# Kernel optimization log

Hardware: AMD Instinct MI355X
Metric: run time of the kernel (lower is better)

The kernel has to match this reference:

```python
import jax, jax.numpy as jnp
import numpy as np

TOP_K = 4  # top_k_neighbors from __init__


def setup_inputs() -> dict:
    key = jax.random.key(0)
    k1, k2, k3, k4 = jax.random.split(key, 4)
    R, B, D, N = 256, 64, 512, 16
    h = jax.random.normal(k1, (R, B, D), dtype=jnp.float32)
    nbrs = jax.random.randint(k2, (R, N), 0, R, dtype=jnp.int32)
    W_msg = jax.random.normal(k3, (D, D), dtype=jnp.float32) * 0.02
    b_msg = jnp.zeros((D,), dtype=jnp.float32)
    W_merge = jax.random.normal(k4, (D, 2 * D), dtype=jnp.float32) * 0.02
    b_merge = jnp.zeros((D,), dtype=jnp.float32)
    return {
        "h_by_region": h,
        "neighbor_indices": nbrs,
        "W_msg": W_msg,
        "b_msg": b_msg,
        "W_merge": W_merge,
        "b_merge": b_merge,
    }


def reference(h_by_region, neighbor_indices, W_msg, b_msg, W_merge, b_merge):
    # h_by_region: [R, B, D]; neighbor_indices: [R, N] int32
    R, B, D = h_by_region.shape
    h = h_by_region
    # sim(r, j) = mean over (B, D) of h[r] * h[j]. Compute the full Gram once
    # ([R, R], tiny) instead of materializing [R, N, B, D] just for sims.
    G = jnp.einsum('rbd,sbd->rs', h, h) / (B * D)
    sims = jnp.take_along_axis(G, neighbor_indices, axis=1)           # [R, N]
    _, top = jax.lax.top_k(sims, TOP_K)                               # [R, K]
    sel = jnp.take_along_axis(neighbor_indices, top, axis=1)          # [R, K]
    # Gather selected neighbor states, project to messages, average over K.
    h_sel = h[sel]                                                    # [R, K, B, D]
    msgs = jnp.einsum('rkbd,ed->rkbe', h_sel, W_msg) + b_msg          # [R, K, B, D]
    m = msgs.mean(axis=1)                                             # [R, B, D]
    cat = jnp.concatenate([h, m], axis=-1)                            # [R, B, 2D]
    out = jnp.einsum('rbf,ef->rbe', cat, W_merge) + b_merge           # [R, B, D]
    avg_fanin = jnp.float32(TOP_K)  # every region keeps exactly top_k neighbors
    return out, avg_fanin
```

## Files before the change

### kernel.cpp

```cpp
#include <hip/hip_runtime.h>
#include <hip/hip_bf16.h>

#define R_ 256
#define B_ 64
#define D_ 512
#define N_ 16
#define K_ 4
#define RBD (B_ * D_)
#define OUT_ELEMS (R_ * B_ * D_)
#define M_TOT (R_ * B_)
#define GSLICES 64
#define GPAIRS 10
#define GBLK (GSLICES * GPAIRS)

typedef __attribute__((address_space(1))) unsigned int g_u32;
typedef __attribute__((address_space(3))) unsigned int l_u32;
using f32x4 = __attribute__((ext_vector_type(4))) float;
using f16x8 = __attribute__((ext_vector_type(8))) _Float16;
using f16x4 = __attribute__((ext_vector_type(4))) _Float16;

__constant__ int kBx[GPAIRS] = {0, 0, 0, 0, 1, 1, 1, 2, 2, 3};
__constant__ int kBy[GPAIRS] = {0, 1, 2, 3, 1, 2, 3, 2, 3, 3};

__global__ __launch_bounds__(256, 4) void gramx_kernel(
    const float* __restrict__ h, const float* __restrict__ Wm,
    const float* __restrict__ Wmsg, _Float16* __restrict__ A16,
    float* __restrict__ Cp, float* __restrict__ W2p) {
  __shared__ char smem[32768];
  const int t = threadIdx.x;
  const int bid = blockIdx.x;

  if (bid >= GBLK) {
    const int gid = bid - GBLK;
    const int db = (gid & 15) * 32;
    const int eb = ((gid >> 4) & 15) * 32;
    const int kc = gid >> 8;
    float(*As)[33] = (float(*)[33])smem;
    float(*Bs)[33] = (float(*)[33])(smem + 32 * 33 * 4);
    const int tx = t % 16, ty = t / 16;
    const int lr = t / 8;
    const int lc = (t % 8) * 4;
    float a00 = 0.f, a01 = 0.f, a10 = 0.f, a11 = 0.f;
    for (int c0 = kc * 128; c0 < kc * 128 + 128; c0 += 32) {
      float4 av = *(const float4*)&Wm[(size_t)(eb + lr) * 1024 + 512 + c0 + lc];
      float4 bv = *(const float4*)&Wmsg[(size_t)(c0 + lr) * 512 + db + lc];
      As[lr][lc + 0] = av.x; As[lr][lc + 1] = av.y;
      As[lr][lc + 2] = av.z; As[lr][lc + 3] = av.w;
      Bs[lr][lc + 0] = bv.x; Bs[lr][lc + 1] = bv.y;
      Bs[lr][lc + 2] = bv.z; Bs[lr][lc + 3] = bv.w;
      __syncthreads();
#pragma unroll
      for (int kk = 0; kk < 32; kk++) {
        float x0 = As[2 * ty + 0][kk], x1 = As[2 * ty + 1][kk];
        float y0 = Bs[kk][2 * tx + 0], y1 = Bs[kk][2 * tx + 1];
        a00 += x0 * y0; a01 += x0 * y1;
        a10 += x1 * y0; a11 += x1 * y1;
      }
      __syncthreads();
    }
    float* base = W2p + (size_t)kc * 512 * 512;
    base[(size_t)(eb + 2 * ty + 0) * 512 + db + 2 * tx + 0] = a00;
    base[(size_t)(eb + 2 * ty + 0) * 512 + db + 2 * tx + 1] = a01;
    base[(size_t)(eb + 2 * ty + 1) * 512 + db + 2 * tx + 0] = a10;
    base[(size_t)(eb + 2 * ty + 1) * 512 + db + 2 * tx + 1] = a11;
    return;
  }

  const int work = (bid & 7) * (GBLK / 8) + (bid >> 3);
  const int s = work / GPAIRS;
  const int pr = work % GPAIRS;
  const int bx = kBx[pr];
  const int by = kBy[pr];
  const int I = bx * 64;
  const int J = by * 64;
  const bool duty = (bx == by);
  const int lane = t & 63;
  const int w = t >> 6;
  char* sHiI = smem;
  char* sHiJ = smem + 8192;
  char* sLoJ = smem + 16384;
  char* sLoI = smem + 24576;
  const int wm = w >> 1, wn = w & 1;
  const int rlane = lane & 15;
  const int kq = lane >> 4;

  f32x4 c1[2][2] = {};
  f32x4 c2[2][2] = {};
  f32x4 c3[2][2] = {};

  const float* hI = h + (size_t)I * RBD + (size_t)s * 512;
  const float* hJ = h + (size_t)J * RBD + (size_t)s * 512;
  const int frow = t >> 4;
  const int fc4 = t & 15;

  float4 rI[4], rJ[4];
#pragma unroll
  for (int u = 0; u < 4; ++u) {
    const int row = u * 16 + frow;
    rI[u] = *(const float4*)&hI[(size_t)row * RBD + fc4 * 4];
    rJ[u] = *(const float4*)&hJ[(size_t)row * RBD + fc4 * 4];
  }

  for (int kt = 0; kt < 8; ++kt) {
    if (kt) __syncthreads();
#pragma unroll
    for (int u = 0; u < 4; ++u) {
      const int row = u * 16 + frow;
      const int boff =
          row * 128 + (((fc4 >> 1) ^ (row & 7)) << 4) + (fc4 & 1) * 8;
      float4 vI = rI[u];
      f16x4 hiI = {(_Float16)vI.x, (_Float16)vI.y, (_Float16)vI.z,
                   (_Float16)vI.w};
      f16x4 loI = {(_Float16)(vI.x - (float)hiI[0]),
                   (_Float16)(vI.y - (float)hiI[1]),
                   (_Float16)(vI.z - (float)hiI[2]),
                   (_Float16)(vI.w - (float)hiI[3])};
      *(f16x4*)(sHiI + boff) = hiI;
      *(f16x4*)(sLoI + boff) = loI;
      float4 vJ = rJ[u];
      f16x4 hiJ = {(_Float16)vJ.x, (_Float16)vJ.y, (_Float16)vJ.z,
                   (_Float16)vJ.w};
      f16x4 loJ = {(_Float16)(vJ.x - (float)hiJ[0]),
                   (_Float16)(vJ.y - (float)hiJ[1]),
                   (_Float16)(vJ.z - (float)hiJ[2]),
                   (_Float16)(vJ.w - (float)hiJ[3])};
      *(f16x4*)(sHiJ + boff) = hiJ;
      *(f16x4*)(sLoJ + boff) = loJ;
      if (duty)
        *(f16x4*)&A16[(size_t)(J + row) * RBD + (size_t)s * 512 + kt * 64 +
                      fc4 * 4] = hiJ;
    }
    __syncthreads();
    if (kt < 7) {
#pragma unroll
      for (int u = 0; u < 4; ++u) {
        const int row = u * 16 + frow;
        rI[u] =
            *(const float4*)&hI[(size_t)row * RBD + (kt + 1) * 64 + fc4 * 4];
        rJ[u] =
            *(const float4*)&hJ[(size_t)row * RBD + (kt + 1) * 64 + fc4 * 4];
      }
    }
#pragma unroll
    for (int ks = 0; ks < 2; ++ks) {
      f16x8 ai[2], li[2], bj[2], lj[2];
#pragma unroll
      for (int i = 0; i < 2; ++i) {
        const int row = wm * 32 + i * 16 + rlane;
        const int slot = (ks * 4 + kq) ^ (row & 7);
        ai[i] = *(const f16x8*)(sHiI + row * 128 + slot * 16);
        li[i] = *(const f16x8*)(sLoI + row * 128 + slot * 16);
      }
#pragma unroll
      for (int j = 0; j < 2; ++j) {
        const int row = wn * 32 + j * 16 + rlane;
        const int slot = (ks * 4 + kq) ^ (row & 7);
        bj[j] = *(const f16x8*)(sHiJ + row * 128 + slot * 16);
        lj[j] = *(const f16x8*)(sLoJ + row * 128 + slot * 16);
      }
#pragma unroll
      for (int i = 0; i < 2; ++i)
#pragma unroll
        for (int j = 0; j < 2; ++j) {
          c1[i][j] = __builtin_amdgcn_mfma_f32_16x16x32_f16(ai[i], bj[j],
                                                            c1[i][j], 0, 0, 0);
          c2[i][j] = __builtin_amdgcn_mfma_f32_16x16x32_f16(ai[i], lj[j],
                                                            c2[i][j], 0, 0, 0);
          c3[i][j] = __builtin_amdgcn_mfma_f32_16x16x32_f16(li[i], bj[j],
                                                            c3[i][j], 0, 0, 0);
        }
    }
  }

  f32x4 cs[2][2];
#pragma unroll
  for (int i = 0; i < 2; ++i)
#pragma unroll
    for (int j = 0; j < 2; ++j)
      cs[i][j] = c1[i][j] + c2[i][j] + c3[i][j];

#pragma unroll
  for (int i = 0; i < 2; ++i) {
#pragma unroll
    for (int reg = 0; reg < 4; ++reg) {
      const int gr = I + wm * 32 + i * 16 + kq * 4 + reg;
      const size_t base = ((size_t)s * 256 + gr) * 256 + J + wn * 32 + rlane;
#pragma unroll
      for (int j = 0; j < 2; ++j) Cp[base + j * 16] = cs[i][j][reg];
    }
  }
  if (!duty) {
#pragma unroll
    for (int i = 0; i < 2; ++i)
#pragma unroll
      for (int j = 0; j < 2; ++j) {
        const int gc = J + wn * 32 + j * 16 + rlane;
        const int gr0 = I + wm * 32 + i * 16 + kq * 4;
        *(f32x4*)&Cp[((size_t)s * 256 + gc) * 256 + gr0] = cs[i][j];
      }
  }
}

__global__ __launch_bounds__(256) void fin_kernel(
    const float* __restrict__ Cp, const int* __restrict__ nbrs,
    const float* __restrict__ W2p, const float* __restrict__ Wm,
    const float* __restrict__ b_msg, const float* __restrict__ b_merge,
    int* __restrict__ sel, float* __restrict__ fanin,
    _Float16* __restrict__ W16, float* __restrict__ bias_eff) {
  const int bx = blockIdx.x;
  const int t = threadIdx.x;
  if (bx < 256) {
    const int r = bx;
    __shared__ float sims_all[256];
    __shared__ int nb_s[N_];
    const float* base = Cp + (size_t)r * 256 + t;
    float acc = 0.f;
#pragma unroll 8
    for (int s = 0; s < GSLICES; ++s) acc += base[(size_t)s * 65536];
    sims_all[t] = acc;
    if (t < N_) nb_s[t] = nbrs[r * N_ + t];
    __syncthreads();
    if (t == 0) {
      float sims_s[N_];
#pragma unroll
      for (int n = 0; n < N_; ++n) sims_s[n] = sims_all[nb_s[n]];
      unsigned used = 0;
#pragma unroll
      for (int k = 0; k < K_; k++) {
        float best = -3.0e38f;
        int bi = 0;
        for (int nn = 0; nn < N_; nn++) {
          if (used & (1u << nn)) continue;
          float vv = sims_s[nn];
          if (vv > best) { best = vv; bi = nn; }
        }
        used |= 1u << bi;
        sel[r * K_ + k] = nb_s[bi];
      }
      if (r == 0) *fanin = 4.0f;
    }
  } else if (bx < 1280) {
    const int i = (bx - 256) * 256 + t;
    const int e = i >> 9;
    const int d = i & 511;
    float acc = 0.f;
#pragma unroll
    for (int kc = 0; kc < 4; ++kc)
      acc += W2p[(size_t)kc * 512 * 512 + (size_t)e * 512 + d];
    W16[(size_t)e * 1024 + 512 + d] = (_Float16)acc;
  } else if (bx < 1536) {
    const int i = (bx - 1280) * 256 + t;
    const int e = i >> 7;
    const int c4 = (i & 127) * 4;
    float4 v = *(const float4*)&Wm[(size_t)e * 1024 + c4];
    f16x4 o = {(_Float16)v.x, (_Float16)v.y, (_Float16)v.z, (_Float16)v.w};
    *(f16x4*)&W16[(size_t)e * 1024 + c4] = o;
  } else {
    const int e = (bx - 1536) * 256 + t;
    const float4* bp = (const float4*)b_msg;
    const float4* wp = (const float4*)&Wm[(size_t)e * 1024 + 512];
    float acc = 0.f;
    for (int c = 0; c < 128; c++) {
      float4 b4 = bp[c], w4 = wp[c];
      acc += b4.x * w4.x + b4.y * w4.y + b4.z * w4.z + b4.w * w4.w;
    }
    bias_eff[e] = acc + b_merge[e];
  }
}

__global__ __launch_bounds__(256, 4) void mfma_gemm_kernel(
    const _Float16* __restrict__ A16, const int* __restrict__ sel,
    const _Float16* __restrict__ W16, const float* __restrict__ bias,
    float* __restrict__ out) {
  const int t = threadIdx.x;
  const int lane = t & 63;
  const int w = t >> 6;
  const int bid = blockIdx.x;
  const int work = (bid & 7) * 128 + (bid >> 3);
  const int eb = (work & 3) * 128;
  const int my = work >> 2;
  const int m0 = my * 64;
  __shared__ char smemA[64 * 128];
  __shared__ char smemW[128 * 128];
  __shared__ int sel_s[4];
  const int wm = w >> 1, wn = w & 1;
  const int rlane = lane & 15;
  const int kq = lane >> 4;

  if (t < 4) sel_s[t] = sel[my * 4 + t];
  __syncthreads();

  f32x4 acc[2][4] = {};

  const char* Ab = (const char*)A16;
  const char* Wb = (const char*)W16;
  const _Float16* g0 = A16 + (size_t)sel_s[0] * RBD;
  const _Float16* g1 = A16 + (size_t)sel_s[1] * RBD;
  const _Float16* g2 = A16 + (size_t)sel_s[2] * RBD;
  const _Float16* g3 = A16 + (size_t)sel_s[3] * RBD;

  for (int kt = 0; kt < 16; ++kt) {
    if (kt < 8) {
#pragma unroll
      for (int u = 0; u < 2; ++u) {
        const int f = u * 256 + t;
        const int row = f >> 3;
        const int slot = (f & 7) ^ (row & 7);
        const char* ga =
            Ab + ((size_t)(m0 + row) * 1024 + kt * 128 + slot * 16);
        char* la = smemA + u * 4096 + w * 1024;
        __builtin_amdgcn_global_load_lds((const g_u32*)ga, (l_u32*)la, 16, 0,
                                         0);
      }
    } else {
      const int kk8 = kt - 8;
#pragma unroll
      for (int u = 0; u < 2; ++u) {
        const int f = u * 256 + t;
        const int row = f >> 3;
        const int slot = f & 7;
        const size_t off = (size_t)row * 512 + kk8 * 64 + slot * 8;
        f16x8 q0 = *(const f16x8*)&g0[off];
        f16x8 q1 = *(const f16x8*)&g1[off];
        f16x8 q2 = *(const f16x8*)&g2[off];
        f16x8 q3 = *(const f16x8*)&g3[off];
        f16x8 m = ((q0 + q1) + (q2 + q3)) * (_Float16)0.25f;
        *(f16x8*)(smemA + row * 128 + ((slot ^ (row & 7)) << 4)) = m;
      }
    }
#pragma unroll
    for (int q = 0; q < 4; ++q) {
      const int f = q * 256 + t;
      const int row = f >> 3;
      const int slot = (f & 7) ^ (row & 7);
      const char* gw = Wb + ((size_t)(eb + row) * 2048 + kt * 128 + slot * 16);
      char* lw = smemW + q * 4096 + w * 1024;
      __builtin_amdgcn_global_load_lds((const g_u32*)gw, (l_u32*)lw, 16, 0, 0);
    }
    __syncthreads();
#pragma unroll
    for (int ks = 0; ks < 2; ++ks) {
      f16x8 a[2], b[4];
#pragma unroll
      for (int i = 0; i < 2; ++i) {
        const int row = wm * 32 + i * 16 + rlane;
        const int slot = (ks * 4 + kq) ^ (row & 7);
        a[i] = *(const f16x8*)(smemA + row * 128 + slot * 16);
      }
#pragma unroll
      for (int j = 0; j < 4; ++j) {
        const int row = wn * 64 + j * 16 + rlane;
        const int slot = (ks * 4 + kq) ^ (row & 7);
        b[j] = *(const f16x8*)(smemW + row * 128 + slot * 16);
      }
#pragma unroll
      for (int i = 0; i < 2; ++i)
#pragma unroll
        for (int j = 0; j < 4; ++j)
          acc[i][j] = __builtin_amdgcn_mfma_f32_16x16x32_f16(a[i], b[j],
                                                             acc[i][j], 0, 0, 0);
    }
    __syncthreads();
  }

  float bj[4];
#pragma unroll
  for (int j = 0; j < 4; ++j) bj[j] = bias[eb + wn * 64 + j * 16 + rlane];
#pragma unroll
  for (int i = 0; i < 2; ++i) {
#pragma unroll
    for (int reg = 0; reg < 4; ++reg) {
      const size_t m = (size_t)m0 + wm * 32 + i * 16 + kq * 4 + reg;
      float* po = out + m * 512 + eb + wn * 64 + rlane;
#pragma unroll
      for (int j = 0; j < 4; ++j) po[j * 16] = acc[i][j][reg] + bj[j];
    }
  }
}

__global__ __launch_bounds__(256) void bias_kernel(
    const float* __restrict__ Wm, const float* __restrict__ b_msg,
    const float* __restrict__ b_merge, float* __restrict__ bias_eff) {
  const int e = blockIdx.x * 256 + threadIdx.x;
  const float4* bp = (const float4*)b_msg;
  const float4* wp = (const float4*)&Wm[(size_t)e * 1024 + 512];
  float acc = 0.f;
  for (int c = 0; c < 128; c++) {
    float4 b4 = bp[c], w4 = wp[c];
    acc += b4.x * w4.x + b4.y * w4.y + b4.z * w4.z + b4.w * w4.w;
  }
  bias_eff[e] = acc + b_merge[e];
}

__global__ __launch_bounds__(256) void sims_topk_kernel(
    const float* __restrict__ h, const int* __restrict__ nbrs,
    int* __restrict__ sel, float* __restrict__ fanin) {
  const int r = blockIdx.x;
  const int t = threadIdx.x;
  const int lane = t & 63;
  const int wave = t >> 6;
  __shared__ float sims_s[N_];
  __shared__ int nb_s[N_];
  if (t < N_) nb_s[t] = nbrs[r * N_ + t];
  __syncthreads();
  const int n0 = wave * 4;
  const float4* hr  = (const float4*)(h + (size_t)r * RBD);
  const float4* hn0 = (const float4*)(h + (size_t)nb_s[n0 + 0] * RBD);
  const float4* hn1 = (const float4*)(h + (size_t)nb_s[n0 + 1] * RBD);
  const float4* hn2 = (const float4*)(h + (size_t)nb_s[n0 + 2] * RBD);
  const float4* hn3 = (const float4*)(h + (size_t)nb_s[n0 + 3] * RBD);
  float a0 = 0.f, a1 = 0.f, a2 = 0.f, a3 = 0.f;
  for (int i = lane; i < RBD / 4; i += 64) {
    float4 x = hr[i];
    float4 y0 = hn0[i], y1 = hn1[i], y2 = hn2[i], y3 = hn3[i];
    a0 += x.x * y0.x + x.y * y0.y + x.z * y0.z + x.w * y0.w;
    a1 += x.x * y1.x + x.y * y1.y + x.z * y1.z + x.w * y1.w;
    a2 += x.x * y2.x + x.y * y2.y + x.z * y2.z + x.w * y2.w;
    a3 += x.x * y3.x + x.y * y3.y + x.z * y3.z + x.w * y3.w;
  }
  float v[4] = {a0, a1, a2, a3};
#pragma unroll
  for (int n = 0; n < 4; n++) {
    float x = v[n];
#pragma unroll
    for (int off = 32; off > 0; off >>= 1) x += __shfl_down(x, off);
    if (lane == 0) sims_s[n0 + n] = x;
  }
  __syncthreads();
  if (t == 0) {
    unsigned used = 0;
#pragma unroll
    for (int k = 0; k < K_; k++) {
      float best = -3.0e38f;
      int bi = 0;
      for (int n = 0; n < N_; n++) {
        if (used & (1u << n)) continue;
        float vv = sims_s[n];
        if (vv > best) { best = vv; bi = n; }
      }
      used |= 1u << bi;
      sel[r * K_ + k] = nb_s[bi];
    }
    if (r == 0) *fanin = 4.0f;
  }
}

__global__ __launch_bounds__(256) void w2eff_f32_kernel(
    const float* __restrict__ Wm, const float* __restrict__ Wmsg,
    float* __restrict__ W2) {
  __shared__ float As[32][33];
  __shared__ float Bs[32][33];
  const int t = threadIdx.x;
  const int eb = blockIdx.y * 32;
  const int db = blockIdx.x * 32;
  const int tx = t % 16, ty = t / 16;
  const int lr = t / 8;
  const int lc = (t % 8) * 4;
  float a00 = 0.f, a01 = 0.f, a10 = 0.f, a11 = 0.f;
  for (int c0 = 0; c0 < 512; c0 += 32) {
    float4 av = *(const float4*)&Wm[(size_t)(eb + lr) * 1024 + 512 + c0 + lc];
    float4 bv = *(const float4*)&Wmsg[(size_t)(c0 + lr) * 512 + db + lc];
    As[lr][lc + 0] = av.x; As[lr][lc + 1] = av.y;
    As[lr][lc + 2] = av.z; As[lr][lc + 3] = av.w;
    Bs[lr][lc + 0] = bv.x; Bs[lr][lc + 1] = bv.y;
    Bs[lr][lc + 2] = bv.z; Bs[lr][lc + 3] = bv.w;
    __syncthreads();
#pragma unroll
    for (int kk = 0; kk < 32; kk++) {
      float x0 = As[2 * ty + 0][kk], x1 = As[2 * ty + 1][kk];
      float y0 = Bs[kk][2 * tx + 0], y1 = Bs[kk][2 * tx + 1];
      a00 += x0 * y0; a01 += x0 * y1;
      a10 += x1 * y0; a11 += x1 * y1;
    }
    __syncthreads();
  }
  W2[(size_t)(eb + 2 * ty + 0) * 512 + db + 2 * tx + 0] = a00;
  W2[(size_t)(eb + 2 * ty + 0) * 512 + db + 2 * tx + 1] = a01;
  W2[(size_t)(eb + 2 * ty + 1) * 512 + db + 2 * tx + 0] = a10;
  W2[(size_t)(eb + 2 * ty + 1) * 512 + db + 2 * tx + 1] = a11;
}

__global__ __launch_bounds__(256) void fused_gemm_f32_kernel(
    const float* __restrict__ h, const int* __restrict__ sel,
    const float* __restrict__ Wm, const float* __restrict__ W2,
    const float* __restrict__ bias_eff, float* __restrict__ out) {
  const int r = blockIdx.y;
  const int eb = blockIdx.x * 256;
  const int t = threadIdx.x;
  __shared__ float As[64][33];
  __shared__ float Ws[256][33];
  __shared__ int sel_s[K_];
  if (t < K_) sel_s[t] = sel[r * K_ + t];
  __syncthreads();
  const size_t hr = (size_t)r * RBD;
  const size_t s0 = (size_t)sel_s[0] * RBD;
  const size_t s1 = (size_t)sel_s[1] * RBD;
  const size_t s2 = (size_t)sel_s[2] * RBD;
  const size_t s3 = (size_t)sel_s[3] * RBD;
  const int tb = t % 8;
  const int te = t / 8;
  const int ab = t / 4;
  const int ac = (t % 4) * 8;
  float acc[8][8] = {};
  for (int d0 = 0; d0 < 1024; d0 += 32) {
    if (d0 < 512) {
      const float* src = h + hr + (size_t)ab * 512 + d0 + ac;
      float4 v0 = *(const float4*)(src);
      float4 v1 = *(const float4*)(src + 4);
      As[ab][ac + 0] = v0.x; As[ab][ac + 1] = v0.y;
      As[ab][ac + 2] = v0.z; As[ab][ac + 3] = v0.w;
      As[ab][ac + 4] = v1.x; As[ab][ac + 5] = v1.y;
      As[ab][ac + 6] = v1.z; As[ab][ac + 7] = v1.w;
    } else {
      const size_t off = (size_t)ab * 512 + (d0 - 512) + ac;
      const float* p0 = h + s0 + off;
      const float* p1 = h + s1 + off;
      const float* p2 = h + s2 + off;
      const float* p3 = h + s3 + off;
      float4 q0 = *(const float4*)p0, q0b = *(const float4*)(p0 + 4);
      float4 q1 = *(const float4*)p1, q1b = *(const float4*)(p1 + 4);
      float4 q2 = *(const float4*)p2, q2b = *(const float4*)(p2 + 4);
      float4 q3 = *(const float4*)p3, q3b = *(const float4*)(p3 + 4);
      As[ab][ac + 0] = 0.25f * (q0.x + q1.x + q2.x + q3.x);
      As[ab][ac + 1] = 0.25f * (q0.y + q1.y + q2.y + q3.y);
      As[ab][ac + 2] = 0.25f * (q0.z + q1.z + q2.z + q3.z);
      As[ab][ac + 3] = 0.25f * (q0.w + q1.w + q2.w + q3.w);
      As[ab][ac + 4] = 0.25f * (q0b.x + q1b.x + q2b.x + q3b.x);
      As[ab][ac + 5] = 0.25f * (q0b.y + q1b.y + q2b.y + q3b.y);
      As[ab][ac + 6] = 0.25f * (q0b.z + q1b.z + q2b.z + q3b.z);
      As[ab][ac + 7] = 0.25f * (q0b.w + q1b.w + q2b.w + q3b.w);
    }
    {
      const float* src = (d0 < 512)
          ? (Wm + (size_t)(eb + t) * 1024 + d0)
          : (W2 + (size_t)(eb + t) * 512 + (d0 - 512));
#pragma unroll
      for (int j = 0; j < 8; j++) {
        float4 v = *(const float4*)(src + 4 * j);
        Ws[t][4 * j + 0] = v.x; Ws[t][4 * j + 1] = v.y;
        Ws[t][4 * j + 2] = v.z; Ws[t][4 * j + 3] = v.w;
      }
    }
    __syncthreads();
#pragma unroll
    for (int kk = 0; kk < 32; kk++) {
      float a[8], wv[8];
#pragma unroll
      for (int i = 0; i < 8; i++) a[i] = As[tb + 8 * i][kk];
#pragma unroll
      for (int j = 0; j < 8; j++) wv[j] = Ws[te + 32 * j][kk];
#pragma unroll
      for (int i = 0; i < 8; i++)
#pragma unroll
        for (int j = 0; j < 8; j++) acc[i][j] += a[i] * wv[j];
    }
    __syncthreads();
  }
  float be[8];
#pragma unroll
  for (int j = 0; j < 8; j++) be[j] = bias_eff[eb + te + 32 * j];
#pragma unroll
  for (int i = 0; i < 8; i++) {
    const int b = tb + 8 * i;
#pragma unroll
    for (int j = 0; j < 8; j++) {
      const int e = eb + te + 32 * j;
      out[hr + (size_t)b * 512 + e] = acc[i][j] + be[j];
    }
  }
}

extern "C" void kernel_launch(void* const* d_in, const int* in_sizes, int n_in,
                              void* d_out, int out_size, void* d_ws,
                              size_t ws_size, hipStream_t stream) {
  const float* h       = (const float*)d_in[0];
  const int*   nbrs    = (const int*)d_in[1];
  const float* W_msg   = (const float*)d_in[2];
  const float* b_msg   = (const float*)d_in[3];
  const float* W_merge = (const float*)d_in[4];
  const float* b_merge = (const float*)d_in[5];
  float* out = (float*)d_out;
  char* ws = (char*)d_ws;

  const size_t SZ_PART = (size_t)GSLICES * 256 * 256 * 4;
  const size_t SZ_A = (size_t)M_TOT * 512 * 2;
  const size_t SZ_W = (size_t)512 * 1024 * 2;
  const size_t SZ_W2P = (size_t)4 * 512 * 512 * 4;
  size_t off = 0;
  int*      sel      = (int*)(ws + off);      off += 4096;
  float*    bias_eff = (float*)(ws + off);    off += 4096;
  float*    Cp       = (float*)(ws + off);    off += SZ_PART;
  _Float16* A16      = (_Float16*)(ws + off); off += SZ_A;
  _Float16* W16      = (_Float16*)(ws + off); off += SZ_W;
  float*    W2p      = (float*)(ws + off);    off += SZ_W2P;
  const size_t NEED = off;

  if (ws_size >= NEED) {
    gramx_kernel<<<GBLK + 1024, 256, 0, stream>>>(h, W_merge, W_msg, A16, Cp,
                                                  W2p);
    fin_kernel<<<1538, 256, 0, stream>>>(Cp, nbrs, W2p, W_merge, b_msg,
                                         b_merge, sel, out + OUT_ELEMS, W16,
                                         bias_eff);
    mfma_gemm_kernel<<<1024, 256, 0, stream>>>(A16, sel, W16, bias_eff, out);
  } else {
    int*   fsel     = (int*)ws;
    float* W2       = (float*)(ws + 4096);
    float* fbias    = (float*)(ws + 4096 + 512 * 512 * 4);
    sims_topk_kernel<<<R_, 256, 0, stream>>>(h, nbrs, fsel, out + OUT_ELEMS);
    bias_kernel<<<2, 256, 0, stream>>>(W_merge, b_msg, b_merge, fbias);
    w2eff_f32_kernel<<<dim3(16, 16), 256, 0, stream>>>(W_merge, W_msg, W2);
    fused_gemm_f32_kernel<<<dim3(2, R_), 256, 0, stream>>>(h, fsel, W_merge,
                                                           W2, fbias, out);
  }
}
```

Baseline: 81.64 us.

## Precompute neighbor-mean activations in fin kernel, load via LDS DMA in GEMM

Moves the averaging of the four selected neighbor fp16 states out of the GEMM main loop and into the fin kernel, writing a materialized mean tensor Am16. The GEMM then streams both halves of K through global_load_lds instead of register loads plus VALU averaging for the second half. Each region's mean is computed once rather than once per output column block (4x redundancy), but this costs an extra 16 MB write and read plus a larger workspace, and the 256 top-k blocks in fin_kernel now do much more serial work.

Result: no change. 80.21 us (-1.8%).

```diff
diff --git a/kernel.cpp b/kernel.cpp
--- a/kernel.cpp
+++ b/kernel.cpp
@@ -205,6 +205,7 @@
     const float* __restrict__ Cp, const int* __restrict__ nbrs,
     const float* __restrict__ W2p, const float* __restrict__ Wm,
     const float* __restrict__ b_msg, const float* __restrict__ b_merge,
+    const _Float16* __restrict__ A16, _Float16* __restrict__ Am16,
     int* __restrict__ sel, float* __restrict__ fanin,
     _Float16* __restrict__ W16, float* __restrict__ bias_eff) {
   const int bx = blockIdx.x;
@@ -213,6 +214,7 @@
     const int r = bx;
     __shared__ float sims_all[256];
     __shared__ int nb_s[N_];
+    __shared__ int sel_sm[K_];
     const float* base = Cp + (size_t)r * 256 + t;
     float acc = 0.f;
 #pragma unroll 8
@@ -235,9 +237,27 @@
           if (vv > best) { best = vv; bi = nn; }
         }
         used |= 1u << bi;
-        sel[r * K_ + k] = nb_s[bi];
+        const int sj = nb_s[bi];
+        sel[r * K_ + k] = sj;
+        sel_sm[k] = sj;
       }
       if (r == 0) *fanin = 4.0f;
+    }
+    __syncthreads();
+    const _Float16* g0 = A16 + (size_t)sel_sm[0] * RBD;
+    const _Float16* g1 = A16 + (size_t)sel_sm[1] * RBD;
+    const _Float16* g2 = A16 + (size_t)sel_sm[2] * RBD;
+    const _Float16* g3 = A16 + (size_t)sel_sm[3] * RBD;
+    _Float16* dst = Am16 + (size_t)r * RBD;
+#pragma unroll 4
+    for (int i = t; i < RBD / 8; i += 256) {
+      const size_t off = (size_t)i * 8;
+      f16x8 q0 = *(const f16x8*)&g0[off];
+      f16x8 q1 = *(const f16x8*)&g1[off];
+      f16x8 q2 = *(const f16x8*)&g2[off];
+      f16x8 q3 = *(const f16x8*)&g3[off];
+      f16x8 m = ((q0 + q1) + (q2 + q3)) * (_Float16)0.25f;
+      *(f16x8*)&dst[off] = m;
     }
   } else if (bx < 1280) {
     const int i = (bx - 256) * 256 + t;
@@ -269,7 +289,7 @@
 }
 
 __global__ __launch_bounds__(256, 4) void mfma_gemm_kernel(
-    const _Float16* __restrict__ A16, const int* __restrict__ sel,
+    const _Float16* __restrict__ A16, const _Float16* __restrict__ Am16,
     const _Float16* __restrict__ W16, const float* __restrict__ bias,
     float* __restrict__ out) {
   const int t = threadIdx.x;
@@ -282,51 +302,28 @@
   const int m0 = my * 64;
   __shared__ char smemA[64 * 128];
   __shared__ char smemW[128 * 128];
-  __shared__ int sel_s[4];
   const int wm = w >> 1, wn = w & 1;
   const int rlane = lane & 15;
   const int kq = lane >> 4;
 
-  if (t < 4) sel_s[t] = sel[my * 4 + t];
-  __syncthreads();
-
   f32x4 acc[2][4] = {};
 
   const char* Ab = (const char*)A16;
+  const char* Amb = (const char*)Am16;
   const char* Wb = (const char*)W16;
-  const _Float16* g0 = A16 + (size_t)sel_s[0] * RBD;
-  const _Float16* g1 = A16 + (size_t)sel_s[1] * RBD;
-  const _Float16* g2 = A16 + (size_t)sel_s[2] * RBD;
-  const _Float16* g3 = A16 + (size_t)sel_s[3] * RBD;
 
   for (int kt = 0; kt < 16; ++kt) {
-    if (kt < 8) {
-#pragma unroll
-      for (int u = 0; u < 2; ++u) {
-        const int f = u * 256 + t;
-        const int row = f >> 3;
-        const int slot = (f & 7) ^ (row & 7);
-        const char* ga =
-            Ab + ((size_t)(m0 + row) * 1024 + kt * 128 + slot * 16);
-        char* la = smemA + u * 4096 + w * 1024;
-        __builtin_amdgcn_global_load_lds((const g_u32*)ga, (l_u32*)la, 16, 0,
-                                         0);
-      }
-    } else {
-      const int kk8 = kt - 8;
-#pragma unroll
-      for (int u = 0; u < 2; ++u) {
-        const int f = u * 256 + t;
-        const int row = f >> 3;
-        const int slot = f & 7;
-        const size_t off = (size_t)row * 512 + kk8 * 64 + slot * 8;
-        f16x8 q0 = *(const f16x8*)&g0[off];
-        f16x8 q1 = *(const f16x8*)&g1[off];
-        f16x8 q2 = *(const f16x8*)&g2[off];
-        f16x8 q3 = *(const f16x8*)&g3[off];
-        f16x8 m = ((q0 + q1) + (q2 + q3)) * (_Float16)0.25f;
-        *(f16x8*)(smemA + row * 128 + ((slot ^ (row & 7)) << 4)) = m;
-      }
+#pragma unroll
+    for (int u = 0; u < 2; ++u) {
+      const int f = u * 256 + t;
+      const int row = f >> 3;
+      const int slot = (f & 7) ^ (row & 7);
+      const char* ga =
+          (kt < 8)
+              ? Ab + ((size_t)(m0 + row) * 1024 + kt * 128 + slot * 16)
+              : Amb + ((size_t)(m0 + row) * 1024 + (kt - 8) * 128 + slot * 16);
+      char* la = smemA + u * 4096 + w * 1024;
+      __builtin_amdgcn_global_load_lds((const g_u32*)ga, (l_u32*)la, 16, 0, 0);
     }
 #pragma unroll
     for (int q = 0; q < 4; ++q) {
@@ -591,6 +588,7 @@
   float*    bias_eff = (float*)(ws + off);    off += 4096;
   float*    Cp       = (float*)(ws + off);    off += SZ_PART;
   _Float16* A16      = (_Float16*)(ws + off); off += SZ_A;
+  _Float16* Am16     = (_Float16*)(ws + off); off += SZ_A;
   _Float16* W16      = (_Float16*)(ws + off); off += SZ_W;
   float*    W2p      = (float*)(ws + off);    off += SZ_W2P;
   const size_t NEED = off;
@@ -599,9 +597,9 @@
     gramx_kernel<<<GBLK + 1024, 256, 0, stream>>>(h, W_merge, W_msg, A16, Cp,
                                                   W2p);
     fin_kernel<<<1538, 256, 0, stream>>>(Cp, nbrs, W2p, W_merge, b_msg,
-                                         b_merge, sel, out + OUT_ELEMS, W16,
-                                         bias_eff);
-    mfma_gemm_kernel<<<1024, 256, 0, stream>>>(A16, sel, W16, bias_eff, out);
+                                         b_merge, A16, Am16, sel,
+                                         out + OUT_ELEMS, W16, bias_eff);
+    mfma_gemm_kernel<<<1024, 256, 0, stream>>>(A16, Am16, W16, bias_eff, out);
   } else {
     int*   fsel     = (int*)ws;
     float* W2       = (float*)(ws + 4096);
```
